# Performance work log

Measured on AMD Instinct MI355X. Metric: run time of the kernel, lower is better.

## Reference

```python
import jax, jax.numpy as jnp
import numpy as np

H = 2048      # hidden_size
I = 4096      # intermediate_size
N = 128       # ssm state_size
HEADS = 64
P = 64        # head_dim
K = 4         # conv kernel
CHUNK = 256
DT_MIN, DT_MAX = 0.0, 100.0
EPS = 1e-5


def segsum(x):
    # x: (..., T) -> (..., T, T) with out[i, j] = sum_{k=j+1..i} x[k], -inf above diag
    T = x.shape[-1]
    cs = jnp.cumsum(x, axis=-1)
    d = cs[..., :, None] - cs[..., None, :]
    mask = jnp.tril(jnp.ones((T, T), dtype=bool))
    return jnp.where(mask, d, -jnp.inf)


def setup_inputs() -> dict:
    key = jax.random.key(0)
    ks = jax.random.split(key, 8)
    return {
        "hidden_states": jax.random.normal(ks[0], (2, 4096, H), jnp.float32),
        "in_proj_w": jax.random.normal(ks[1], (2 * (I + N) + HEADS, H), jnp.float32) * 0.02,
        "conv_w": jax.random.normal(ks[2], (I + 2 * N, 1, K), jnp.float32) * 0.2,
        "conv_b": jax.random.normal(ks[3], (I + 2 * N,), jnp.float32) * 0.02,
        "dt_bias": jax.random.uniform(ks[4], (HEADS,), jnp.float32),
        "A_log": jnp.log(jax.random.uniform(ks[5], (HEADS,), jnp.float32, 1.0, 16.0)),
        "D": jnp.ones((HEADS,), jnp.float32),
        "norm_w": jnp.ones((I,), jnp.float32),
        "out_proj_w": jax.random.normal(ks[6], (H, I), jnp.float32) * 0.02,
    }


def reference(hidden_states, in_proj_w, conv_w, conv_b, dt_bias, A_log, D, norm_w, out_proj_w):
    b, l, _ = hidden_states.shape
    # in_proj -> [z (I), xBC (I+2N), dt (HEADS)]  (d_mlp == 0 with these dims)
    zxbcdt = hidden_states @ in_proj_w.T
    z, xBC, dt = jnp.split(zxbcdt, [I, I + (I + 2 * N)], axis=-1)

    # causal depthwise conv1d + SiLU
    conv = jax.lax.conv_general_dilated(
        xBC.transpose(0, 2, 1), conv_w, (1,), [(K - 1, 0)],
        dimension_numbers=("NCH", "OIH", "NCH"), feature_group_count=I + 2 * N)
    xBC = jax.nn.silu((conv + conv_b[None, :, None]).transpose(0, 2, 1))
    x, B, C = jnp.split(xBC, [I, I + N], axis=-1)

    A = -jnp.exp(A_log)                                        # (h,)
    dt = jnp.clip(jax.nn.softplus(dt + dt_bias), DT_MIN, DT_MAX)  # (b,l,h)

    # SSD chunked scan (groups = 1 for B/C)
    X = x.reshape(b, l, HEADS, P) * dt[..., None]              # x * dt
    Adt = dt * A                                               # (b,l,h)
    c = l // CHUNK
    Xc = X.reshape(b, c, CHUNK, HEADS, P)
    Bc = B.reshape(b, c, CHUNK, N)
    Cc = C.reshape(b, c, CHUNK, N)
    Ac = Adt.reshape(b, c, CHUNK, HEADS).transpose(0, 3, 1, 2)  # (b,h,c,cl)
    A_cum = jnp.cumsum(Ac, axis=-1)

    # intra-chunk (diagonal) contribution
    L = jnp.exp(segsum(Ac))                                    # (b,h,c,cl,cl)
    Y_diag = jnp.einsum("bcln,bcsn,bhcls,bcshp->bclhp", Cc, Bc, L, Xc)

    # chunk states and inter-chunk recurrence
    decay_states = jnp.exp(A_cum[..., -1:] - A_cum)            # (b,h,c,cl)
    states = jnp.einsum("bcln,bhcl,bclhp->bchpn", Bc, decay_states, Xc)
    states = jnp.concatenate([jnp.zeros_like(states[:, :1]), states], axis=1)
    chunk_A = jnp.pad(A_cum[..., -1], ((0, 0), (0, 0), (1, 0)))  # (b,h,c+1)
    decay_chunk = jnp.exp(segsum(chunk_A))                     # (b,h,c+1,c+1)
    new_states = jnp.einsum("bhzc,bchpn->bzhpn", decay_chunk, states)
    prev_states = new_states[:, :-1]                           # (b,c,h,p,n)

    Y_off = jnp.einsum("bcln,bchpn,bhcl->bclhp", Cc, prev_states, jnp.exp(A_cum))
    y = (Y_diag + Y_off).reshape(b, l, HEADS, P)
    y = y + x.reshape(b, l, HEADS, P) * D[None, None, :, None]  # skip (D term)
    y = y.reshape(b, l, I)

    # gated RMSNorm (norm_before_gate=True): normalize, gate by silu(z), scale
    yf = y.astype(jnp.float32)
    yf = yf * jax.lax.rsqrt(jnp.mean(yf * yf, axis=-1, keepdims=True) + EPS)
    yf = yf * jax.nn.silu(z.astype(jnp.float32))
    y = (norm_w * yf).astype(hidden_states.dtype)

    return y @ out_proj_w.T
```

## Files before the change

kernel.cpp:

```cpp
#include <hip/hip_runtime.h>

typedef unsigned short u16;
typedef __attribute__((ext_vector_type(8))) short bfx8;
typedef __attribute__((ext_vector_type(4))) float f32x4;
typedef __attribute__((ext_vector_type(4))) unsigned short u16x4;

__device__ __forceinline__ float bf2f(u16 u){ return __builtin_bit_cast(float, (unsigned)u << 16); }
__device__ __forceinline__ u16 f2bf(float f){
  unsigned u = __builtin_bit_cast(unsigned, f);
  return (u16)((u + 0x7fffu + ((u >> 16) & 1u)) >> 16);
}

__device__ __forceinline__ void gload_lds16(const void* g, void* l){
  __builtin_amdgcn_global_load_lds((const __attribute__((address_space(1))) void*)g,
                                   (__attribute__((address_space(3))) void*)l, 16, 0, 0);
}

__global__ __launch_bounds__(256) void cvt_kernel(const float* __restrict__ in, u16* __restrict__ out, int n4){
  int i = blockIdx.x * 256 + threadIdx.x;
  if (i >= n4) return;
  f32x4 v = *(const f32x4*)&in[(long)i * 4];
  u16x4 o = { f2bf(v[0]), f2bf(v[1]), f2bf(v[2]), f2bf(v[3]) };
  *(u16x4*)&out[(long)i * 4] = o;
}

__global__ __launch_bounds__(256) void cvt2_kernel(const float* __restrict__ a, u16* __restrict__ oa, int na4,
                                                   const float* __restrict__ b2, u16* __restrict__ ob, int nb4){
  int i = blockIdx.x * 256 + threadIdx.x;
  const float* src; u16* dst; int idx;
  if (i < na4){ src = a; dst = oa; idx = i; }
  else { idx = i - na4; if (idx >= nb4) return; src = b2; dst = ob; }
  f32x4 v = *(const f32x4*)&src[(long)idx * 4];
  u16x4 o = { f2bf(v[0]), f2bf(v[1]), f2bf(v[2]), f2bf(v[3]) };
  *(u16x4*)&dst[(long)idx * 4] = o;
}

template<int F32OUT>
__global__ __launch_bounds__(512, 2)
void gemm256(const u16* __restrict__ A, const u16* __restrict__ W,
             void* __restrict__ out0, void* __restrict__ out1,
             int K, int ld0, int ld1, int nsplit)
{
  __shared__ __align__(16) u16 SA[2][16384];
  __shared__ __align__(16) u16 SB[2][16384];
  const int tid = threadIdx.x;
  const int wid = tid >> 6, lane = tid & 63;
  const int wr = wid >> 2, wc = wid & 3;
  const int bm = blockIdx.x, bn = blockIdx.y;
  const int rr = lane & 15, kg = lane >> 4;
  const int NT = K >> 6;

  const int srow = tid >> 3;
  const int ssw = ((tid & 7) * 16) ^ ((srow & 7) << 4);
  const u16* gA = A + ((long)bm * 256 + srow) * K + (ssw >> 1);
  const u16* gB = W + ((long)bn * 256 + srow) * K + (ssw >> 1);
  const long r64 = (long)64 * K;
  const int dst = tid * 8;

#define STAGE_A(t, ht) { const u16* s_ = gA + (long)(ht) * 2 * r64 + ((t) << 6); \
    gload_lds16(s_,       &SA[(t) & 1][(ht) * 8192 + dst]); \
    gload_lds16(s_ + r64, &SA[(t) & 1][(ht) * 8192 + 4096 + dst]); }
#define STAGE_B(t, ht) { const u16* s_ = gB + (long)(ht) * 2 * r64 + ((t) << 6); \
    gload_lds16(s_,       &SB[(t) & 1][(ht) * 8192 + dst]); \
    gload_lds16(s_ + r64, &SB[(t) & 1][(ht) * 8192 + 4096 + dst]); }

  const int swr = (rr & 7) << 4;
  const int ca0 = ((kg * 16) ^ swr) >> 1;
  const int ca1 = ((64 + kg * 16) ^ swr) >> 1;
  int bA[8], bB[4];
#pragma unroll
  for (int j = 0; j < 8; j++) bA[j] = ((2 * j + wr) * 16 + rr) * 64;
#pragma unroll
  for (int i = 0; i < 4; i++) bB[i] = ((4 * i + wc) * 16 + rr) * 64;

  f32x4 acc[8][4] = {};

  STAGE_A(0, 0); STAGE_A(0, 1); STAGE_B(0, 0); STAGE_B(0, 1);
  if (NT > 1) STAGE_A(1, 0);
  asm volatile("s_waitcnt vmcnt(2)" ::: "memory");
  asm volatile("s_barrier" ::: "memory");

  for (int u = 0; u < NT; ++u){
    const int p = u & 1;
    bfx8 bf[4][2];
#pragma unroll
    for (int k = 0; k < 4; ++k){
      bfx8 af[2][2];
#pragma unroll
      for (int jj = 0; jj < 2; jj++){
        const int base = bA[2 * k + jj];
        af[jj][0] = *(const bfx8*)&SA[p][base + ca0];
        af[jj][1] = *(const bfx8*)&SA[p][base + ca1];
      }
      if (k == 0){
#pragma unroll
        for (int i = 0; i < 4; i++){
          bf[i][0] = *(const bfx8*)&SB[p][bB[i] + ca0];
          bf[i][1] = *(const bfx8*)&SB[p][bB[i] + ca1];
        }
        if (u + 1 < NT) { STAGE_B(u + 1, 0); STAGE_B(u + 1, 1); }
      }
      else if (k == 1) { if (u + 1 < NT) STAGE_A(u + 1, 1); }
      else if (k == 3) {
        if (u + 2 < NT)      { STAGE_A(u + 2, 0); asm volatile("s_waitcnt vmcnt(2)" ::: "memory"); }
        else if (u + 1 < NT) { asm volatile("s_waitcnt vmcnt(0)" ::: "memory"); }
      }
      asm volatile("s_barrier" ::: "memory");
      __builtin_amdgcn_s_setprio(1);
#pragma unroll
      for (int jj = 0; jj < 2; jj++)
#pragma unroll
        for (int i = 0; i < 4; i++){
          acc[2 * k + jj][i] = __builtin_amdgcn_mfma_f32_16x16x32_bf16(af[jj][0], bf[i][0], acc[2 * k + jj][i], 0, 0, 0);
          acc[2 * k + jj][i] = __builtin_amdgcn_mfma_f32_16x16x32_bf16(af[jj][1], bf[i][1], acc[2 * k + jj][i], 0, 0, 0);
        }
      __builtin_amdgcn_s_setprio(0);
    }
  }
#undef STAGE_A
#undef STAGE_B

  int bn2 = bn; void* op = out0; int ldo = ld0;
  if (bn >= nsplit){ bn2 = bn - nsplit; op = out1; ldo = ld1; }
  const int r4b = (lane >> 4) * 4;
#pragma unroll
  for (int j = 0; j < 8; j++)
#pragma unroll
    for (int i = 0; i < 4; i++)
#pragma unroll
      for (int r4 = 0; r4 < 4; r4++){
        long row = (long)bm * 256 + (2 * j + wr) * 16 + r4b + r4;
        long col = (long)bn2 * 256 + (4 * i + wc) * 16 + rr;
        long idx = row * ldo + col;
        if (F32OUT) ((float*)op)[idx] = acc[j][i][r4];
        else        ((u16*)op)[idx]  = f2bf(acc[j][i][r4]);
      }
}

__global__ __launch_bounds__(256) void dt_kernel(const float* __restrict__ hs, const float* __restrict__ w,
                                                 const float* __restrict__ dt_bias, float* __restrict__ dtp){
  __shared__ float hsS[32][66];
  __shared__ float wS[64][66];
  const int tid = threadIdx.x;
  const int j = tid & 63, rgrp = tid >> 6;
  const long row0 = (long)blockIdx.x * 32;
  const int srow = tid >> 3, sc0 = (tid & 7) * 8;
  const int wrow = tid >> 2, wc0 = (tid & 3) * 16;
  const float* hsg = hs + (row0 + srow) * 2048 + sc0;
  const float* wg  = w + (long)(8448 + wrow) * 2048 + wc0;

  f32x4 acc[8] = {};
  for (int k0 = 0; k0 < 2048; k0 += 64){
    *(f32x4*)&hsS[srow][sc0]     = *(const f32x4*)&hsg[k0];
    *(f32x4*)&hsS[srow][sc0 + 4] = *(const f32x4*)&hsg[k0 + 4];
#pragma unroll
    for (int q = 0; q < 4; q++)
      *(f32x4*)&wS[wrow][wc0 + q * 4] = *(const f32x4*)&wg[k0 + q * 4];
    __syncthreads();
#pragma unroll
    for (int kk = 0; kk < 64; kk += 4){
      f32x4 wv = *(const f32x4*)&wS[j][kk];
#pragma unroll
      for (int r = 0; r < 8; r++){
        f32x4 hv = *(const f32x4*)&hsS[rgrp * 8 + r][kk];
        acc[r] += hv * wv;
      }
    }
    __syncthreads();
  }
  float bias = dt_bias[j];
#pragma unroll
  for (int r = 0; r < 8; r++){
    float x = acc[r][0] + acc[r][1] + acc[r][2] + acc[r][3] + bias;
    float sp = (x > 20.f) ? x : log1pf(expf(x));
    sp = fminf(fmaxf(sp, 0.f), 100.f);
    dtp[(row0 + rgrp * 8 + r) * 64 + j] = sp;
  }
}

__global__ __launch_bounds__(64) void acum_kernel(const float* __restrict__ dtp, const float* __restrict__ A_log,
                                                  float* __restrict__ acum, float* __restrict__ suma){
  int bid = blockIdx.x;
  int c = bid & 15, h = (bid >> 4) & 63, b = bid >> 10;
  int lane = threadIdx.x;
  float Ah = -expf(A_log[h]);
  long base = ((long)(b * 4096 + c * 256)) * 64 + h;
  float v[4]; float s = 0.f;
#pragma unroll
  for (int i = 0; i < 4; i++){ float adt = dtp[base + (lane * 4 + i) * 64] * Ah; s += adt; v[i] = s; }
  float tot = s, run = s;
  for (int off = 1; off < 64; off <<= 1){ float u = __shfl_up(run, off); if (lane >= off) run += u; }
  float excl = run - tot;
  long ob = (long)bid * 256 + lane * 4;
#pragma unroll
  for (int i = 0; i < 4; i++) acum[ob + i] = excl + v[i];
  if (lane == 63) suma[bid] = run;
}

__global__ __launch_bounds__(256) void conv_kernel(const u16* __restrict__ xbc, const float* __restrict__ cw,
                                                   const float* __restrict__ cb,
                                                   u16* __restrict__ xact,
                                                   u16* __restrict__ bmat, u16* __restrict__ cmat){
  int pb = blockIdx.x;
  int l0 = (pb & 1023) * 4;
  long pos0 = ((long)(pb >> 10) << 12) + l0;
  for (int cg = threadIdx.x; cg < 544; cg += 256){
    int ch = cg * 8;
    f32x4 cwv[8];
#pragma unroll
    for (int t = 0; t < 8; t++) cwv[t] = *(const f32x4*)&cw[(ch + t) * 4];
    float cbv[8];
#pragma unroll
    for (int t = 0; t < 8; t++) cbv[t] = cb[ch + t];
    bfx8 rr[7];
    bfx8 zz = {};
    rr[0] = (l0 >= 3) ? *(const bfx8*)&xbc[(pos0 - 3) * 4352 + ch] : zz;
    rr[1] = (l0 >= 2) ? *(const bfx8*)&xbc[(pos0 - 2) * 4352 + ch] : zz;
    rr[2] = (l0 >= 1) ? *(const bfx8*)&xbc[(pos0 - 1) * 4352 + ch] : zz;
#pragma unroll
    for (int q = 0; q < 4; q++) rr[3 + q] = *(const bfx8*)&xbc[(pos0 + q) * 4352 + ch];
#pragma unroll
    for (int li = 0; li < 4; li++){
      bfx8 o;
#pragma unroll
      for (int t = 0; t < 8; t++){
        float a = cbv[t] + cwv[t][0] * bf2f((u16)rr[li][t])     + cwv[t][1] * bf2f((u16)rr[li + 1][t])
                         + cwv[t][2] * bf2f((u16)rr[li + 2][t]) + cwv[t][3] * bf2f((u16)rr[li + 3][t]);
        float val = a / (1.f + expf(-a));
        o[t] = (short)f2bf(val);
      }
      long pos = pos0 + li;
      if (ch < 4096)      *(bfx8*)&xact[pos * 4096 + ch] = o;
      else if (ch < 4224) *(bfx8*)&bmat[pos * 128 + ch - 4096] = o;
      else                *(bfx8*)&cmat[pos * 128 + ch - 4224] = o;
    }
  }
}

__global__ __launch_bounds__(256) void bt_transpose(const u16* __restrict__ bmat, u16* __restrict__ bmatT){
  __shared__ u16 T[128 * 136];
  int bx = blockIdx.x;
  int b = bx >> 5, lt = bx & 31;
  int l0 = lt * 128;
  int tid = threadIdx.x;
  for (int idx = tid; idx < 2048; idx += 256){
    int lrow = idx >> 4, ns = (idx & 15) * 8;
    *(bfx8*)&T[lrow * 136 + ns] = *(const bfx8*)&bmat[((long)b * 4096 + l0 + lrow) * 128 + ns];
  }
  __syncthreads();
  for (int idx = tid; idx < 2048; idx += 256){
    int nrow = idx >> 4, ls = (idx & 15) * 8;
    bfx8 o;
#pragma unroll
    for (int j = 0; j < 8; j++) o[j] = (short)T[(ls + j) * 136 + nrow];
    *(bfx8*)&bmatT[(long)b * 524288 + (long)nrow * 4096 + l0 + ls] = o;
  }
}

__global__ __launch_bounds__(256) void cbt_kernel(const u16* __restrict__ cmat, const u16* __restrict__ bmat,
                                                  float* __restrict__ G){
  int bid = blockIdx.x;
  int ss = bid & 3, bc = bid >> 2;
  int b = bc >> 4, c = bc & 15;
  long rowbase = (long)b * 4096 + c * 256;
  int tid = threadIdx.x, wid = tid >> 6, lane = tid & 63;
  int rr = lane & 15, ko = (lane >> 4) * 8;
  f32x4 acc[4][4] = {};
#pragma unroll
  for (int kk = 0; kk < 4; kk++){
    bfx8 cf[4], bf[4];
#pragma unroll
    for (int lt = 0; lt < 4; lt++) cf[lt] = *(const bfx8*)&cmat[(rowbase + wid * 64 + lt * 16 + rr) * 128 + kk * 32 + ko];
#pragma unroll
    for (int st = 0; st < 4; st++) bf[st] = *(const bfx8*)&bmat[(rowbase + ss * 64 + st * 16 + rr) * 128 + kk * 32 + ko];
#pragma unroll
    for (int lt = 0; lt < 4; lt++)
#pragma unroll
      for (int st = 0; st < 4; st++)
        acc[lt][st] = __builtin_amdgcn_mfma_f32_16x16x32_bf16(cf[lt], bf[st], acc[lt][st], 0, 0, 0);
  }
  long gb2 = (long)bc * 65536;
#pragma unroll
  for (int lt = 0; lt < 4; lt++)
#pragma unroll
    for (int st = 0; st < 4; st++)
#pragma unroll
      for (int r4 = 0; r4 < 4; r4++)
        G[gb2 + (long)(wid * 64 + lt * 16 + (lane >> 4) * 4 + r4) * 256 + ss * 64 + st * 16 + rr] = acc[lt][st][r4];
}

__global__ __launch_bounds__(256, 4) void states_kernel(const u16* __restrict__ xact, const u16* __restrict__ bmatT,
                                                        const float* __restrict__ acum, const float* __restrict__ suma,
                                                        const float* __restrict__ dtp, u16* __restrict__ stR){
  __shared__ __align__(16) u16 XdT[64 * 264];
  __shared__ float fac[256];
  int bid = blockIdx.x;
  int h = bid & 63, c = (bid >> 6) & 15, b = bid >> 10;
  int tid = threadIdx.x;
  long rowbase = (long)b * 4096 + c * 256;
  long aco = ((long)((b * 64 + h) * 16 + c)) * 256;
  float sA = suma[(b * 64 + h) * 16 + c];
  fac[tid] = dtp[(rowbase + tid) * 64 + h] * expf(sA - acum[aco + tid]);
  __syncthreads();
  char* xb = (char*)XdT;
  for (int idx = tid; idx < 2048; idx += 256){
    int l = idx >> 3, ps = (idx & 7) * 8;
    int key = (idx & 7) << 4;
    bfx8 xv = *(const bfx8*)&xact[(rowbase + l) * 4096 + h * 64 + ps];
#pragma unroll
    for (int j = 0; j < 8; j++)
      *(u16*)(xb + ((((ps + j) * 264 + l) * 2) ^ key)) = f2bf(bf2f((u16)xv[j]) * fac[l]);
  }
  __syncthreads();
  int wid = tid >> 6, lane = tid & 63;
  int rr = lane & 15, ko = (lane >> 4) * 8;
  const u16* btb = bmatT + (long)b * 524288 + c * 256;
  const int arow = wid * 16 + rr;
  const int akey = ((arow >> 3) & 7) << 4;
  f32x4 acc[8] = {};
#pragma unroll
  for (int ks = 0; ks < 8; ks++){
    bfx8 a = *(const bfx8*)(xb + (((arow * 264 + ks * 32 + ko) * 2) ^ akey));
#pragma unroll
    for (int nt = 0; nt < 8; nt++){
      bfx8 bb = *(const bfx8*)&btb[(long)(nt * 16 + rr) * 4096 + ks * 32 + ko];
      acc[nt] = __builtin_amdgcn_mfma_f32_16x16x32_bf16(a, bb, acc[nt], 0, 0, 0);
    }
  }
  long ob = (long)bid * 8192;
#pragma unroll
  for (int nt = 0; nt < 8; nt++)
#pragma unroll
    for (int r4 = 0; r4 < 4; r4++){
      int p = wid * 16 + (lane >> 4) * 4 + r4;
      stR[ob + p * 128 + nt * 16 + rr] = f2bf(acc[nt][r4]);
    }
}

__global__ __launch_bounds__(256) void scan_kernel(u16* stR, const float* __restrict__ suma){
  int g = blockIdx.x;
  int s = g & 7, bh = g >> 3;
  int b = bh >> 6, h = bh & 63;
  int tid = threadIdx.x;
  long off0 = (long)s * 1024 + tid * 4;
  f32x4 R = {};
  for (int c = 0; c < 16; c++){
    long base = ((long)((b * 16 + c) * 64 + h)) * 8192 + off0;
    float sc = expf(suma[(b * 64 + h) * 16 + c]);
    u16x4 e4 = *(const u16x4*)&stR[base];
    u16x4 o = { f2bf(R[0]), f2bf(R[1]), f2bf(R[2]), f2bf(R[3]) };
    *(u16x4*)&stR[base] = o;
#pragma unroll
    for (int t = 0; t < 4; t++) R[t] = sc * R[t] + bf2f(e4[t]);
  }
}

__global__ __launch_bounds__(256, 4) void ydiag_kernel(const u16* __restrict__ cmat, const float* __restrict__ G,
                                                       const u16* xact,
                                                       const u16* __restrict__ rbuf, const float* __restrict__ acum,
                                                       const float* __restrict__ dtp,
                                                       const float* __restrict__ Dv, u16* ybuf){
  __shared__ __align__(16) u16 XdTq[64 * 72];
  __shared__ float acL[256];
  __shared__ float dtl[256];
  int bid = blockIdx.x;
  int h = bid & 63, c = (bid >> 6) & 15, b = bid >> 10;
  int tid = threadIdx.x, wid = tid >> 6, lane = tid & 63;
  long rowbase = (long)b * 4096 + c * 256;
  long aco = ((long)((b * 64 + h) * 16 + c)) * 256;
  acL[tid] = acum[aco + tid];
  dtl[tid] = dtp[(rowbase + tid) * 64 + h];
  __syncthreads();

  int rr = lane & 15, ko = (lane >> 4) * 8;
  f32x4 acc[4][4] = {};

  long rb = (long)bid * 8192;
#pragma unroll
  for (int kk = 0; kk < 4; kk++){
    bfx8 cf[4];
#pragma unroll
    for (int lt = 0; lt < 4; lt++)
      cf[lt] = *(const bfx8*)&cmat[(rowbase + wid * 64 + lt * 16 + rr) * 128 + kk * 32 + ko];
#pragma unroll
    for (int pt = 0; pt < 4; pt++){
      bfx8 bb = *(const bfx8*)&rbuf[rb + (pt * 16 + rr) * 128 + kk * 32 + ko];
#pragma unroll
      for (int lt = 0; lt < 4; lt++) acc[lt][pt] = __builtin_amdgcn_mfma_f32_16x16x32_bf16(cf[lt], bb, acc[lt][pt], 0, 0, 0);
    }
  }
#pragma unroll
  for (int lt = 0; lt < 4; lt++)
#pragma unroll
    for (int r4 = 0; r4 < 4; r4++){
      float e = expf(acL[wid * 64 + lt * 16 + (lane >> 4) * 4 + r4]);
#pragma unroll
      for (int pt = 0; pt < 4; pt++) acc[lt][pt][r4] *= e;
    }

  char* xqb = (char*)XdTq;
  const long gb2 = (long)((b * 16 + c)) * 65536;
  const int nsp = 2 * (wid + 1);
  for (int q = 0; q < 4; q++){
    __syncthreads();
    for (int idx = tid; idx < 512; idx += 256){
      int lq = idx >> 3, ps = (idx & 7) * 8;
      int key = (idx & 7) << 4;
      int l = q * 64 + lq;
      bfx8 xv = *(const bfx8*)&xact[(rowbase + l) * 4096 + h * 64 + ps];
#pragma unroll
      for (int j = 0; j < 8; j++)
        *(u16*)(xqb + ((((ps + j) * 72 + lq) * 2) ^ key)) = f2bf(bf2f((u16)xv[j]) * dtl[l]);
    }
    __syncthreads();
#pragma unroll
    for (int sub = 0; sub < 2; sub++){
      int sp = q * 2 + sub;
      if (sp >= nsp) continue;
      int s0 = sp * 32;
#pragma unroll
      for (int lt = 0; lt < 4; lt++){
        int lrow = wid * 64 + lt * 16 + rr;
        float eL = acL[lrow];
        f32x4 g0 = *(const f32x4*)&G[gb2 + (long)lrow * 256 + s0 + ko];
        f32x4 g1 = *(const f32x4*)&G[gb2 + (long)lrow * 256 + s0 + ko + 4];
        bfx8 a1;
#pragma unroll
        for (int j = 0; j < 4; j++){
          int s = s0 + ko + j;
          float sc = (s <= lrow) ? expf(eL - acL[s]) : 0.f;
          a1[j] = (short)f2bf(g0[j] * sc);
        }
#pragma unroll
        for (int j = 0; j < 4; j++){
          int s = s0 + ko + 4 + j;
          float sc = (s <= lrow) ? expf(eL - acL[s]) : 0.f;
          a1[4 + j] = (short)f2bf(g1[j] * sc);
        }
#pragma unroll
        for (int pt = 0; pt < 4; pt++){
          int prow = pt * 16 + rr;
          bfx8 bb = *(const bfx8*)(xqb + (((prow * 72 + sub * 32 + ko) * 2) ^ (((prow >> 3) & 7) << 4)));
          acc[lt][pt] = __builtin_amdgcn_mfma_f32_16x16x32_bf16(a1, bb, acc[lt][pt], 0, 0, 0);
        }
      }
    }
  }
  float Dh = Dv[h];
#pragma unroll
  for (int lt = 0; lt < 4; lt++)
#pragma unroll
    for (int pt = 0; pt < 4; pt++)
#pragma unroll
      for (int r4 = 0; r4 < 4; r4++){
        int lrow = wid * 64 + lt * 16 + (lane >> 4) * 4 + r4;
        int pcol = pt * 16 + rr;
        long gi = (rowbase + lrow) * 4096 + h * 64 + pcol;
        ybuf[gi] = f2bf(acc[lt][pt][r4] + bf2f(xact[gi]) * Dh);
      }
}

__global__ __launch_bounds__(256) void rms_kernel(const u16* ybuf, const u16* zbuf,
                                                  const float* __restrict__ norm_w, u16* ynorm){
  __shared__ float red[4];
  long row = blockIdx.x;
  int tid = threadIdx.x;
  long yb = row * 4096 + tid * 16;
  bfx8 v0 = *(const bfx8*)&ybuf[yb];
  bfx8 v1 = *(const bfx8*)&ybuf[yb + 8];
  float vals[16];
#pragma unroll
  for (int t = 0; t < 8; t++){ vals[t] = bf2f((u16)v0[t]); vals[8 + t] = bf2f((u16)v1[t]); }
  float ss = 0.f;
#pragma unroll
  for (int t = 0; t < 16; t++) ss += vals[t] * vals[t];
#pragma unroll
  for (int off = 32; off >= 1; off >>= 1) ss += __shfl_xor(ss, off);
  if ((tid & 63) == 0) red[tid >> 6] = ss;
  __syncthreads();
  float rs = rsqrtf((red[0] + red[1] + red[2] + red[3]) * (1.f / 4096.f) + 1e-5f);
  bfx8 z0 = *(const bfx8*)&zbuf[yb];
  bfx8 z1 = *(const bfx8*)&zbuf[yb + 8];
  bfx8 o0, o1;
#pragma unroll
  for (int t = 0; t < 16; t++){
    float zv = bf2f((u16)(t < 8 ? z0[t] : z1[t - 8]));
    float g = zv / (1.f + expf(-zv));
    u16 r = f2bf(vals[t] * rs * norm_w[tid * 16 + t] * g);
    if (t < 8) o0[t] = (short)r; else o1[t - 8] = (short)r;
  }
  *(bfx8*)&ynorm[yb] = o0;
  *(bfx8*)&ynorm[yb + 8] = o1;
}

extern "C" void kernel_launch(void* const* d_in, const int* in_sizes, int n_in,
                              void* d_out, int out_size, void* d_ws, size_t ws_size,
                              hipStream_t stream){
  const float* hs   = (const float*)d_in[0];
  const float* inw  = (const float*)d_in[1];
  const float* cw   = (const float*)d_in[2];
  const float* cb   = (const float*)d_in[3];
  const float* dtb  = (const float*)d_in[4];
  const float* alog = (const float*)d_in[5];
  const float* Dv   = (const float*)d_in[6];
  const float* nw   = (const float*)d_in[7];
  const float* outw = (const float*)d_in[8];

  const size_t REQ = 147857408ULL;
  if (ws_size < REQ){
    hipMemsetAsync(d_out, 0x42, (size_t)out_size * 4, stream);
    return;
  }
  char* ws = (char*)d_ws;
  u16*   hsb  = (u16*)  (ws + 0L);
  u16*   wbi  = (u16*)  (ws + 33554432L);
  u16*   xbc  = (u16*)  (ws + 68157440L);
  u16*   xact = (u16*)  (ws + 0L);
  u16*   stR  = (u16*)  (ws + 68157440L);
  u16*   wbo  = (u16*)  (ws + 101711872L);
  u16*   bmatT= (u16*)  (ws + 118489088L);
  float* Gbuf = (float*)(ws + 120586240L);
  float* dtp  = (float*)(ws + 139460608L);
  float* acum = (float*)(ws + 141557760L);
  float* suma = (float*)(ws + 143654912L);
  u16*   bmat = (u16*)  (ws + 143663104L);
  u16*   cmat = (u16*)  (ws + 145760256L);
  u16*   zbuf = (u16*)  d_out;

  cvt2_kernel<<<33280, 256, 0, stream>>>(hs, hsb, 4194304, inw, wbi, 4325376);
  gemm256<0><<<dim3(32, 33), 512, 0, stream>>>(hsb, wbi, zbuf, xbc, 2048, 4096, 4352, 16);
  dt_kernel<<<256, 256, 0, stream>>>(hs, inw, dtb, dtp);
  acum_kernel<<<2048, 64, 0, stream>>>(dtp, alog, acum, suma);
  conv_kernel<<<2048, 256, 0, stream>>>(xbc, cw, cb, xact, bmat, cmat);
  cvt_kernel<<<8192, 256, 0, stream>>>(outw, wbo, 2097152);
  bt_transpose<<<64, 256, 0, stream>>>(bmat, bmatT);
  cbt_kernel<<<128, 256, 0, stream>>>(cmat, bmat, Gbuf);
  states_kernel<<<2048, 256, 0, stream>>>(xact, bmatT, acum, suma, dtp, stR);
  scan_kernel<<<1024, 256, 0, stream>>>(stR, suma);
  ydiag_kernel<<<2048, 256, 0, stream>>>(cmat, Gbuf, xact, stR, acum, dtp, Dv, xact);
  rms_kernel<<<8192, 256, 0, stream>>>(xact, zbuf, nw, xact);
  gemm256<1><<<dim3(32, 8), 512, 0, stream>>>(xact, wbo, d_out, d_out, 4096, 2048, 2048, 999);
}
```

Before: 903.9 us.

## Fuse hidden-state bf16 cast into dt kernel, widen conv rows, balance ydiag warps

The fp32-to-bf16 conversion of the hidden states moves into dt_kernel, which already reads those values. This removes one full read pass over the input, and the separate cast kernel now handles only the weights. The conv kernel processes 8 positions per block instead of 4, cutting the redundant halo loads. The ydiag kernel pairs a low and a high row band per warp so the causal triangular work is spread evenly across warps instead of being skewed toward the last warp.

Result: no change. 918.1 us (+1.6%).

```diff
diff --git a/kernel.cpp b/kernel.cpp
--- a/kernel.cpp
+++ b/kernel.cpp
@@ -22,17 +22,6 @@
   f32x4 v = *(const f32x4*)&in[(long)i * 4];
   u16x4 o = { f2bf(v[0]), f2bf(v[1]), f2bf(v[2]), f2bf(v[3]) };
   *(u16x4*)&out[(long)i * 4] = o;
-}
-
-__global__ __launch_bounds__(256) void cvt2_kernel(const float* __restrict__ a, u16* __restrict__ oa, int na4,
-                                                   const float* __restrict__ b2, u16* __restrict__ ob, int nb4){
-  int i = blockIdx.x * 256 + threadIdx.x;
-  const float* src; u16* dst; int idx;
-  if (i < na4){ src = a; dst = oa; idx = i; }
-  else { idx = i - na4; if (idx >= nb4) return; src = b2; dst = ob; }
-  f32x4 v = *(const f32x4*)&src[(long)idx * 4];
-  u16x4 o = { f2bf(v[0]), f2bf(v[1]), f2bf(v[2]), f2bf(v[3]) };
-  *(u16x4*)&dst[(long)idx * 4] = o;
 }
 
 template<int F32OUT>
@@ -138,7 +127,8 @@
 }
 
 __global__ __launch_bounds__(256) void dt_kernel(const float* __restrict__ hs, const float* __restrict__ w,
-                                                 const float* __restrict__ dt_bias, float* __restrict__ dtp){
+                                                 const float* __restrict__ dt_bias, float* __restrict__ dtp,
+                                                 u16* __restrict__ hsb){
   __shared__ float hsS[32][66];
   __shared__ float wS[64][66];
   const int tid = threadIdx.x;
@@ -151,8 +141,14 @@
 
   f32x4 acc[8] = {};
   for (int k0 = 0; k0 < 2048; k0 += 64){
-    *(f32x4*)&hsS[srow][sc0]     = *(const f32x4*)&hsg[k0];
-    *(f32x4*)&hsS[srow][sc0 + 4] = *(const f32x4*)&hsg[k0 + 4];
+    f32x4 va = *(const f32x4*)&hsg[k0];
+    f32x4 vb = *(const f32x4*)&hsg[k0 + 4];
+    *(f32x4*)&hsS[srow][sc0]     = va;
+    *(f32x4*)&hsS[srow][sc0 + 4] = vb;
+    u16x4 oa = { f2bf(va[0]), f2bf(va[1]), f2bf(va[2]), f2bf(va[3]) };
+    u16x4 ob = { f2bf(vb[0]), f2bf(vb[1]), f2bf(vb[2]), f2bf(vb[3]) };
+    *(u16x4*)&hsb[(row0 + srow) * 2048 + k0 + sc0]     = oa;
+    *(u16x4*)&hsb[(row0 + srow) * 2048 + k0 + sc0 + 4] = ob;
 #pragma unroll
     for (int q = 0; q < 4; q++)
       *(f32x4*)&wS[wrow][wc0 + q * 4] = *(const f32x4*)&wg[k0 + q * 4];
@@ -202,8 +198,8 @@
                                                    u16* __restrict__ xact,
                                                    u16* __restrict__ bmat, u16* __restrict__ cmat){
   int pb = blockIdx.x;
-  int l0 = (pb & 1023) * 4;
-  long pos0 = ((long)(pb >> 10) << 12) + l0;
+  int l0 = (pb & 511) * 8;
+  long pos0 = ((long)(pb >> 9) << 12) + l0;
   for (int cg = threadIdx.x; cg < 544; cg += 256){
     int ch = cg * 8;
     f32x4 cwv[8];
@@ -212,15 +208,15 @@
     float cbv[8];
 #pragma unroll
     for (int t = 0; t < 8; t++) cbv[t] = cb[ch + t];
-    bfx8 rr[7];
+    bfx8 rr[11];
     bfx8 zz = {};
     rr[0] = (l0 >= 3) ? *(const bfx8*)&xbc[(pos0 - 3) * 4352 + ch] : zz;
     rr[1] = (l0 >= 2) ? *(const bfx8*)&xbc[(pos0 - 2) * 4352 + ch] : zz;
     rr[2] = (l0 >= 1) ? *(const bfx8*)&xbc[(pos0 - 1) * 4352 + ch] : zz;
 #pragma unroll
-    for (int q = 0; q < 4; q++) rr[3 + q] = *(const bfx8*)&xbc[(pos0 + q) * 4352 + ch];
-#pragma unroll
-    for (int li = 0; li < 4; li++){
+    for (int q = 0; q < 8; q++) rr[3 + q] = *(const bfx8*)&xbc[(pos0 + q) * 4352 + ch];
+#pragma unroll
+    for (int li = 0; li < 8; li++){
       bfx8 o;
 #pragma unroll
       for (int t = 0; t < 8; t++){
@@ -373,6 +369,11 @@
   __syncthreads();
 
   int rr = lane & 15, ko = (lane >> 4) * 8;
+  int lrow0[4];
+#pragma unroll
+  for (int lt = 0; lt < 4; lt++)
+    lrow0[lt] = (lt < 2) ? (32 * wid + lt * 16) : (32 * (7 - wid) + (lt - 2) * 16);
+
   f32x4 acc[4][4] = {};
 
   long rb = (long)bid * 8192;
@@ -381,7 +382,7 @@
     bfx8 cf[4];
 #pragma unroll
     for (int lt = 0; lt < 4; lt++)
-      cf[lt] = *(const bfx8*)&cmat[(rowbase + wid * 64 + lt * 16 + rr) * 128 + kk * 32 + ko];
+      cf[lt] = *(const bfx8*)&cmat[(rowbase + lrow0[lt] + rr) * 128 + kk * 32 + ko];
 #pragma unroll
     for (int pt = 0; pt < 4; pt++){
       bfx8 bb = *(const bfx8*)&rbuf[rb + (pt * 16 + rr) * 128 + kk * 32 + ko];
@@ -393,14 +394,13 @@
   for (int lt = 0; lt < 4; lt++)
 #pragma unroll
     for (int r4 = 0; r4 < 4; r4++){
-      float e = expf(acL[wid * 64 + lt * 16 + (lane >> 4) * 4 + r4]);
+      float e = expf(acL[lrow0[lt] + (lane >> 4) * 4 + r4]);
 #pragma unroll
       for (int pt = 0; pt < 4; pt++) acc[lt][pt][r4] *= e;
     }
 
   char* xqb = (char*)XdTq;
   const long gb2 = (long)((b * 16 + c)) * 65536;
-  const int nsp = 2 * (wid + 1);
   for (int q = 0; q < 4; q++){
     __syncthreads();
     for (int idx = tid; idx < 512; idx += 256){
@@ -416,11 +416,13 @@
 #pragma unroll
     for (int sub = 0; sub < 2; sub++){
       int sp = q * 2 + sub;
-      if (sp >= nsp) continue;
+      bool doA = (sp <= wid), doB = (sp <= 7 - wid);
+      if (!doA && !doB) continue;
       int s0 = sp * 32;
 #pragma unroll
       for (int lt = 0; lt < 4; lt++){
-        int lrow = wid * 64 + lt * 16 + rr;
+        if (lt < 2 ? !doA : !doB) continue;
+        int lrow = lrow0[lt] + rr;
         float eL = acL[lrow];
         f32x4 g0 = *(const f32x4*)&G[gb2 + (long)lrow * 256 + s0 + ko];
         f32x4 g1 = *(const f32x4*)&G[gb2 + (long)lrow * 256 + s0 + ko + 4];
@@ -453,7 +455,7 @@
     for (int pt = 0; pt < 4; pt++)
 #pragma unroll
       for (int r4 = 0; r4 < 4; r4++){
-        int lrow = wid * 64 + lt * 16 + (lane >> 4) * 4 + r4;
+        int lrow = lrow0[lt] + (lane >> 4) * 4 + r4;
         int pcol = pt * 16 + rr;
         long gi = (rowbase + lrow) * 4096 + h * 64 + pcol;
         ybuf[gi] = f2bf(acc[lt][pt][r4] + bf2f(xact[gi]) * Dh);
@@ -527,11 +529,11 @@
   u16*   cmat = (u16*)  (ws + 145760256L);
   u16*   zbuf = (u16*)  d_out;
 
-  cvt2_kernel<<<33280, 256, 0, stream>>>(hs, hsb, 4194304, inw, wbi, 4325376);
+  cvt_kernel<<<16896, 256, 0, stream>>>(inw, wbi, 4325376);
+  dt_kernel<<<256, 256, 0, stream>>>(hs, inw, dtb, dtp, hsb);
   gemm256<0><<<dim3(32, 33), 512, 0, stream>>>(hsb, wbi, zbuf, xbc, 2048, 4096, 4352, 16);
-  dt_kernel<<<256, 256, 0, stream>>>(hs, inw, dtb, dtp);
   acum_kernel<<<2048, 64, 0, stream>>>(dtp, alog, acum, suma);
-  conv_kernel<<<2048, 256, 0, stream>>>(xbc, cw, cb, xact, bmat, cmat);
+  conv_kernel<<<1024, 256, 0, stream>>>(xbc, cw, cb, xact, bmat, cmat);
   cvt_kernel<<<8192, 256, 0, stream>>>(outw, wbo, 2097152);
   bt_transpose<<<64, 256, 0, stream>>>(bmat, bmatT);
   cbt_kernel<<<128, 256, 0, stream>>>(cmat, bmat, Gbuf);
```
